# Kernel optimization log

Measured on AMD Instinct MI355X. Metric: run time of the kernel, lower is better.

The kernel has to match this reference:

```python
import jax, jax.numpy as jnp
import numpy as np

B, S, H = 1, 2048, 4096
N_HEADS, N_KV, HEAD_DIM = 32, 8, 128
ROPE_THETA = 10000.0


def setup_inputs() -> dict:
    key = jax.random.key(0)
    k1, k2, k3 = jax.random.split(key, 3)
    hidden_states = jax.random.normal(k1, (B, S, H), dtype=jnp.float32)
    # fused QKV projection weight: rows = (n_heads + 2*n_kv_heads) * head_dim
    Wqkv = jax.random.normal(k2, ((N_HEADS + 2 * N_KV) * HEAD_DIM, H), dtype=jnp.float32) * 0.02
    Wo = jax.random.normal(k3, (H, N_HEADS * HEAD_DIM), dtype=jnp.float32) * 0.02
    return {"hidden_states": hidden_states, "Wqkv": Wqkv, "Wo": Wo}


def _rope_tables(seqlen, dim, theta):
    inv_freq = 1.0 / (theta ** (jnp.arange(0, dim, 2, dtype=jnp.float32) / dim))  # [dim/2]
    t = jnp.arange(seqlen, dtype=jnp.float32)
    freqs = jnp.outer(t, inv_freq)  # [S, dim/2]
    return jnp.cos(freqs), jnp.sin(freqs)


def _apply_rope(x, cos, sin):
    # torch code: reshape(...,2,-1).transpose -> view_as_complex pairs (x[j], x[j+d/2])
    # i.e. NeoX rotate-half on first/second halves of head_dim.
    d2 = x.shape[-1] // 2
    x1, x2 = x[..., :d2], x[..., d2:]
    c = cos[None, :, None, :]  # [1,S,1,d/2]
    s = sin[None, :, None, :]
    return jnp.concatenate([x1 * c - x2 * s, x1 * s + x2 * c], axis=-1)


def reference(hidden_states, Wqkv, Wo):
    b, s, h = hidden_states.shape
    # fused QKV projection
    qkv = jnp.einsum('bsh,oh->bso', hidden_states, Wqkv)
    q_end = N_HEADS * HEAD_DIM
    k_end = q_end + N_KV * HEAD_DIM
    xq = qkv[..., :q_end].reshape(b, s, N_HEADS, HEAD_DIM)
    xk = qkv[..., q_end:k_end].reshape(b, s, N_KV, HEAD_DIM)
    xv = qkv[..., k_end:].reshape(b, s, N_KV, HEAD_DIM)
    # RoPE (start_pos = 0 prefill)
    cos, sin = _rope_tables(s, HEAD_DIM, ROPE_THETA)
    xq = _apply_rope(xq, cos, sin)
    xk = _apply_rope(xk, cos, sin)
    # GQA: expand kv heads to query heads (head h uses kv head h // groups)
    groups = N_HEADS // N_KV
    xk = jnp.repeat(xk, groups, axis=2)  # [b,s,nH,hd]
    xv = jnp.repeat(xv, groups, axis=2)
    # causal attention, softmax scale 1/sqrt(head_dim) (flash_attn default, softcap=0)
    scale = 1.0 / jnp.sqrt(jnp.float32(HEAD_DIM))
    scores = jnp.einsum('bqhd,bkhd->bhqk', xq, xk) * scale
    causal = jnp.tril(jnp.ones((s, s), dtype=bool))
    scores = jnp.where(causal[None, None, :, :], scores, jnp.float32(-1e30))
    probs = jax.nn.softmax(scores, axis=-1)
    out = jnp.einsum('bhqk,bkhd->bqhd', probs, xv).reshape(b, s, N_HEADS * HEAD_DIM)
    attn_output = jnp.einsum('bsd,hd->bsh', out, Wo)
    return attn_output
```

## Files before the change

kernel.cpp:

```cpp
#include <hip/hip_runtime.h>
#include <stdint.h>

typedef unsigned short u16;
typedef unsigned int   u32;
typedef short bf16x8 __attribute__((ext_vector_type(8)));
typedef float f32x4  __attribute__((ext_vector_type(4)));

__device__ __forceinline__ u16 f2bf(float f) {
    union { float f; u32 u; } v; v.f = f;
    u32 u = v.u;
    u32 r = (u + 0x7fffu + ((u >> 16) & 1u)) >> 16;
    return (u16)r;
}
__device__ __forceinline__ float bf2f(u16 h) {
    union { u32 u; float f; } v; v.u = ((u32)h) << 16;
    return v.f;
}

__device__ __forceinline__ void gload_lds16(const void* g, void* l) {
    __builtin_amdgcn_global_load_lds(
        (__attribute__((address_space(1))) void*)g,
        (__attribute__((address_space(3))) void*)l,
        16, 0, 0);
}

__global__ __launch_bounds__(256) void cvt_all(const float4* __restrict__ s1, uint2* __restrict__ d1,
                                               const float4* __restrict__ s2, uint2* __restrict__ d2,
                                               const float4* __restrict__ s3, uint2* __restrict__ d3) {
    const float4* s; uint2* d; int i;
    int b = blockIdx.x;
    if (b < 8192)        { s = s1; d = d1; i = b * 256 + threadIdx.x; }
    else if (b < 32768)  { s = s2; d = d2; i = (b - 8192) * 256 + threadIdx.x; }
    else                 { s = s3; d = d3; i = (b - 32768) * 256 + threadIdx.x; }
    float4 v = s[i];
    uint2 o;
    o.x = (u32)f2bf(v.x) | ((u32)f2bf(v.y) << 16);
    o.y = (u32)f2bf(v.z) | ((u32)f2bf(v.w) << 16);
    d[i] = o;
}

template <typename OUT_T>
__global__ __launch_bounds__(256) void gemm_bt(const u16* __restrict__ A,
                                               const u16* __restrict__ B,
                                               OUT_T* __restrict__ C,
                                               int M, int N, int K) {
    __shared__ u16 As[128 * 32];
    __shared__ u16 Bs[128 * 32];

    const int tid  = threadIdx.x;
    const int lane = tid & 63;
    const int wv   = tid >> 6;
    const int row0 = blockIdx.y * 128;
    const int col0 = blockIdx.x * 128;

    const int wm = (wv >> 1) * 64;
    const int wn = (wv & 1) * 64;
    const int fr = lane & 15;
    const int fq = (lane >> 4) * 8;

    const int srow = lane >> 2;
    const int scol = (lane & 3) * 8;

    f32x4 acc[4][4];
#pragma unroll
    for (int i = 0; i < 4; ++i)
#pragma unroll
        for (int j = 0; j < 4; ++j) acc[i][j] = f32x4{0.f, 0.f, 0.f, 0.f};

    for (int k0 = 0; k0 < K; k0 += 32) {
        __syncthreads();
#pragma unroll
        for (int i = 0; i < 2; ++i) {
            const int chunk = wv * 2 + i;
            const int r     = chunk * 16 + srow;
            gload_lds16(A + (size_t)(row0 + r) * K + k0 + scol, &As[r * 32 + scol]);
            gload_lds16(B + (size_t)(col0 + r) * K + k0 + scol, &Bs[r * 32 + scol]);
        }
        __syncthreads();

        bf16x8 af[4], bf[4];
#pragma unroll
        for (int mt = 0; mt < 4; ++mt)
            af[mt] = *(const bf16x8*)&As[(wm + mt * 16 + fr) * 32 + fq];
#pragma unroll
        for (int nt = 0; nt < 4; ++nt)
            bf[nt] = *(const bf16x8*)&Bs[(wn + nt * 16 + fr) * 32 + fq];
#pragma unroll
        for (int mt = 0; mt < 4; ++mt)
#pragma unroll
            for (int nt = 0; nt < 4; ++nt)
                acc[mt][nt] = __builtin_amdgcn_mfma_f32_16x16x32_bf16(
                    af[mt], bf[nt], acc[mt][nt], 0, 0, 0);
    }

    const int orow4 = (lane >> 4) * 4;
    const int ocol  = lane & 15;
#pragma unroll
    for (int mt = 0; mt < 4; ++mt)
#pragma unroll
        for (int nt = 0; nt < 4; ++nt)
#pragma unroll
            for (int r = 0; r < 4; ++r) {
                int mm = row0 + wm + mt * 16 + orow4 + r;
                int nn = col0 + wn + nt * 16 + ocol;
                float v = acc[mt][nt][r];
                if constexpr (sizeof(OUT_T) == 2)
                    C[(size_t)mm * N + nn] = (OUT_T)f2bf(v);
                else
                    C[(size_t)mm * N + nn] = (OUT_T)v;
            }
}

__global__ __launch_bounds__(256) void prep_kv(const u16* __restrict__ qkv,
                                               u16* __restrict__ Kb,
                                               u16* __restrict__ Vt) {
    if (blockIdx.x < 4096) {
        int id = blockIdx.x * 256 + threadIdx.x;
        int d  = id & 63;
        int t  = id >> 6;
        int kh = t & 7;
        int s  = t >> 3;
        const size_t rowbase = (size_t)s * 6144 + 4096;
        float inv = __expf(-(float)d * (9.210340371976184f / 64.0f));
        float ang = (float)s * inv;
        float cs, sn; __sincosf(ang, &sn, &cs);
        float x1 = bf2f(qkv[rowbase + kh * 128 + d]);
        float x2 = bf2f(qkv[rowbase + kh * 128 + d + 64]);
        size_t o = ((size_t)kh * 2048 + s) * 128 + d;
        Kb[o]      = f2bf(x1 * cs - x2 * sn);
        Kb[o + 64] = f2bf(x1 * sn + x2 * cs);
    } else {
        int id = (blockIdx.x - 4096) * 256 + threadIdx.x;
        int s8 = id & 255;
        int d  = (id >> 8) & 127;
        int vh = id >> 15;
        u16 tmp[8];
#pragma unroll
        for (int j = 0; j < 8; ++j)
            tmp[j] = qkv[(size_t)(s8 * 8 + j) * 6144 + 5120 + vh * 128 + d];
        *(uint4*)(Vt + ((size_t)vh * 128 + d) * 2048 + s8 * 8) = *(uint4*)tmp;
    }
}

__device__ __forceinline__ void attn_pass(const bf16x8 qf[4], f32x4 acc[8], float lr[4],
                                          const u16* Ks, const u16* Vs, u16* Psw,
                                          int w, int m, int quad, bool diag, float sl2e) {
    f32x4 sacc[4];
#pragma unroll
    for (int nt = 0; nt < 4; ++nt) sacc[nt] = f32x4{0.f, 0.f, 0.f, 0.f};
#pragma unroll
    for (int kk = 0; kk < 4; ++kk) {
#pragma unroll
        for (int nt = 0; nt < 4; ++nt) {
            int pos = (kk * 4 + quad) ^ (m & 7);
            bf16x8 b = *(const bf16x8*)&Ks[(nt * 16 + m) * 128 + pos * 8];
            sacc[nt] = __builtin_amdgcn_mfma_f32_16x16x32_bf16(qf[kk], b, sacc[nt], 0, 0, 0);
        }
    }

#pragma unroll
    for (int nt = 0; nt < 4; ++nt)
#pragma unroll
        for (int r = 0; r < 4; ++r) {
            float p = __builtin_amdgcn_exp2f(sacc[nt][r] * sl2e);
            if (diag && (nt * 16 + m > w * 16 + quad * 4 + r)) p = 0.f;
            sacc[nt][r] = p;
            lr[r] += p;
        }

#pragma unroll
    for (int nt = 0; nt < 4; ++nt)
#pragma unroll
        for (int r = 0; r < 4; ++r)
            Psw[(quad * 4 + r) * 72 + nt * 16 + m] = f2bf(sacc[nt][r]);

#pragma unroll
    for (int kk2 = 0; kk2 < 2; ++kk2) {
        bf16x8 a = *(const bf16x8*)&Psw[m * 72 + kk2 * 32 + quad * 8];
#pragma unroll
        for (int nt = 0; nt < 8; ++nt) {
            int n = nt * 16 + m;
            int pos = (kk2 * 4 + quad) ^ (m & 7);
            bf16x8 b = *(const bf16x8*)&Vs[n * 64 + pos * 8];
            acc[nt] = __builtin_amdgcn_mfma_f32_16x16x32_bf16(a, b, acc[nt], 0, 0, 0);
        }
    }
}

__global__ __launch_bounds__(256) void attn_mfma(const u16* __restrict__ qkv,
                                                 const u16* __restrict__ Kb,
                                                 const u16* __restrict__ Vt,
                                                 u16* __restrict__ ctx) {
    __shared__ u16 Ks[64 * 128];
    __shared__ u16 Vs[128 * 64];
    __shared__ u16 Ps[4][16 * 72];

    const int tid  = threadIdx.x;
    const int lane = tid & 63;
    const int w    = tid >> 6;
    const int m    = lane & 15;
    const int quad = lane >> 4;
    const int h    = blockIdx.y;
    const int kh   = h >> 2;
    const int qtA  = blockIdx.x;
    const int qtB  = 31 - qtA;

    const u16* Ktile0 = Kb + (size_t)kh * 2048 * 128;
    const u16* Vtile0 = Vt + (size_t)kh * 128 * 2048;
    const float sl2e = 0.08838834764831845f * 1.4426950408889634f;

    bf16x8 qa[4], qb[4];
#pragma unroll
    for (int which = 0; which < 2; ++which) {
        const int qt = which ? qtB : qtA;
        const int s  = qt * 64 + w * 16 + m;
        bf16x8 raw[4];
        const u16* qp = qkv + (size_t)s * 6144 + h * 128 + quad * 8;
#pragma unroll
        for (int kk = 0; kk < 4; ++kk)
            raw[kk] = *(const bf16x8*)(qp + kk * 32);
        bf16x8* dst = which ? qb : qa;
#pragma unroll
        for (int half = 0; half < 2; ++half)
#pragma unroll
            for (int j = 0; j < 8; ++j) {
                int d = half * 32 + quad * 8 + j;
                float inv = __expf(-(float)d * (9.210340371976184f / 64.0f));
                float ang = (float)s * inv;
                float cs, sn; __sincosf(ang, &sn, &cs);
                float x1 = bf2f(((const u16*)&raw[half])[j]);
                float x2 = bf2f(((const u16*)&raw[half + 2])[j]);
                ((u16*)&dst[half])[j]     = f2bf(x1 * cs - x2 * sn);
                ((u16*)&dst[half + 2])[j] = f2bf(x1 * sn + x2 * cs);
            }
    }

    f32x4 accA[8], accB[8];
#pragma unroll
    for (int i = 0; i < 8; ++i) { accA[i] = f32x4{0.f, 0.f, 0.f, 0.f}; accB[i] = f32x4{0.f, 0.f, 0.f, 0.f}; }
    float lA[4] = {0.f, 0.f, 0.f, 0.f};
    float lB[4] = {0.f, 0.f, 0.f, 0.f};

    for (int kt = 0; kt <= qtB; ++kt) {
        __syncthreads();
        {
            const u16* Kt = Ktile0 + (size_t)kt * 64 * 128;
#pragma unroll
            for (int i = 0; i < 4; ++i) {
                int slot = i * 256 + tid;
                int row = slot >> 4, cp = slot & 15;
                int gc = cp ^ (row & 7);
                gload_lds16(Kt + row * 128 + gc * 8, &Ks[slot * 8]);
            }
            const u16* Vtt = Vtile0 + kt * 64;
#pragma unroll
            for (int i = 0; i < 4; ++i) {
                int slot = i * 256 + tid;
                int row = slot >> 3, cp = slot & 7;
                int gc = cp ^ (row & 7);
                gload_lds16(Vtt + (size_t)row * 2048 + gc * 8, &Vs[slot * 8]);
            }
        }
        __syncthreads();

        if (kt <= qtA)
            attn_pass(qa, accA, lA, Ks, Vs, Ps[w], w, m, quad, kt == qtA, sl2e);
        attn_pass(qb, accB, lB, Ks, Vs, Ps[w], w, m, quad, kt == qtB, sl2e);
    }

#pragma unroll
    for (int which = 0; which < 2; ++which) {
        const int qt   = which ? qtB : qtA;
        f32x4*   acc   = which ? accB : accA;
        float*   lr    = which ? lB   : lA;
#pragma unroll
        for (int r = 0; r < 4; ++r) {
            float s_ = lr[r];
            s_ += __shfl_xor(s_, 1);
            s_ += __shfl_xor(s_, 2);
            s_ += __shfl_xor(s_, 4);
            s_ += __shfl_xor(s_, 8);
            lr[r] = s_;
        }
#pragma unroll
        for (int r = 0; r < 4; ++r) {
            float inv = 1.f / lr[r];
            size_t rowg = (size_t)(qt * 64 + w * 16 + quad * 4 + r);
#pragma unroll
            for (int nt = 0; nt < 8; ++nt)
                ctx[rowg * 4096 + h * 128 + nt * 16 + m] = f2bf(acc[nt][r] * inv);
        }
    }
}

extern "C" void kernel_launch(void* const* d_in, const int* in_sizes, int n_in,
                              void* d_out, int out_size, void* d_ws, size_t ws_size,
                              hipStream_t stream) {
    const float* hs   = (const float*)d_in[0];
    const float* wqkv = (const float*)d_in[1];
    const float* wo   = (const float*)d_in[2];
    float* out = (float*)d_out;

    char* ws = (char*)d_ws;
    u16* hA  = (u16*)ws;  ws += (size_t)2048 * 4096 * 2;
    u16* wQ  = (u16*)ws;  ws += (size_t)6144 * 4096 * 2;
    u16* wO  = (u16*)ws;  ws += (size_t)4096 * 4096 * 2;
    u16* qkv = (u16*)ws;  ws += (size_t)2048 * 6144 * 2;
    u16* Kb  = (u16*)ws;  ws += (size_t)8 * 2048 * 128 * 2;
    u16* Vt  = (u16*)ws;  ws += (size_t)8 * 128 * 2048 * 2;
    u16* ctx = (u16*)ws;  ws += (size_t)2048 * 4096 * 2;

    cvt_all<<<49152, 256, 0, stream>>>((const float4*)hs,   (uint2*)hA,
                                       (const float4*)wqkv, (uint2*)wQ,
                                       (const float4*)wo,   (uint2*)wO);

    gemm_bt<u16><<<dim3(48, 16), 256, 0, stream>>>(hA, wQ, qkv, 2048, 6144, 4096);

    prep_kv<<<5120, 256, 0, stream>>>(qkv, Kb, Vt);

    attn_mfma<<<dim3(16, 32), 256, 0, stream>>>(qkv, Kb, Vt, ctx);

    gemm_bt<float><<<dim3(32, 16), 256, 0, stream>>>(ctx, wO, out, 2048, 4096, 4096);
}
```

Measured before the change: 545.5 us.

## Double-buffer LDS tiles in GEMM and attention to overlap loads with MFMA

Both the bf16 GEMM and the attention kernel now keep two LDS buffers for the A/B (or K/V) tiles. The next tile's global-to-LDS async loads are issued right after a single barrier, before computing on the current buffer, so each iteration needs one barrier instead of two. The aim is to hide global memory latency behind the MFMA work. The cost is twice the LDS footprint, which may lower occupancy, especially in attention (about 73KB per block). The overlap may also be lost if the compiler inserts a full vmcnt wait before the LDS reads.

```diff
diff --git a/kernel.cpp b/kernel.cpp
--- a/kernel.cpp
+++ b/kernel.cpp
@@ -44,8 +44,8 @@
                                                const u16* __restrict__ B,
                                                OUT_T* __restrict__ C,
                                                int M, int N, int K) {
-    __shared__ u16 As[128 * 32];
-    __shared__ u16 Bs[128 * 32];
+    __shared__ u16 As[2][128 * 32];
+    __shared__ u16 Bs[2][128 * 32];
 
     const int tid  = threadIdx.x;
     const int lane = tid & 63;
@@ -67,24 +67,32 @@
 #pragma unroll
         for (int j = 0; j < 4; ++j) acc[i][j] = f32x4{0.f, 0.f, 0.f, 0.f};
 
-    for (int k0 = 0; k0 < K; k0 += 32) {
-        __syncthreads();
+    auto stage = [&](int buf, int k0) {
 #pragma unroll
         for (int i = 0; i < 2; ++i) {
             const int chunk = wv * 2 + i;
             const int r     = chunk * 16 + srow;
-            gload_lds16(A + (size_t)(row0 + r) * K + k0 + scol, &As[r * 32 + scol]);
-            gload_lds16(B + (size_t)(col0 + r) * K + k0 + scol, &Bs[r * 32 + scol]);
-        }
+            gload_lds16(A + (size_t)(row0 + r) * K + k0 + scol, &As[buf][r * 32 + scol]);
+            gload_lds16(B + (size_t)(col0 + r) * K + k0 + scol, &Bs[buf][r * 32 + scol]);
+        }
+    };
+
+    const int nk = K >> 5;
+    stage(0, 0);
+
+    for (int ki = 0; ki < nk; ++ki) {
         __syncthreads();
-
+        if (ki + 1 < nk) stage((ki + 1) & 1, (ki + 1) << 5);
+
+        const u16* as = As[ki & 1];
+        const u16* bs = Bs[ki & 1];
         bf16x8 af[4], bf[4];
 #pragma unroll
         for (int mt = 0; mt < 4; ++mt)
-            af[mt] = *(const bf16x8*)&As[(wm + mt * 16 + fr) * 32 + fq];
+            af[mt] = *(const bf16x8*)&as[(wm + mt * 16 + fr) * 32 + fq];
 #pragma unroll
         for (int nt = 0; nt < 4; ++nt)
-            bf[nt] = *(const bf16x8*)&Bs[(wn + nt * 16 + fr) * 32 + fq];
+            bf[nt] = *(const bf16x8*)&bs[(wn + nt * 16 + fr) * 32 + fq];
 #pragma unroll
         for (int mt = 0; mt < 4; ++mt)
 #pragma unroll
@@ -191,8 +199,8 @@
                                                  const u16* __restrict__ Kb,
                                                  const u16* __restrict__ Vt,
                                                  u16* __restrict__ ctx) {
-    __shared__ u16 Ks[64 * 128];
-    __shared__ u16 Vs[128 * 64];
+    __shared__ u16 Ks[2][64 * 128];
+    __shared__ u16 Vs[2][128 * 64];
     __shared__ u16 Ps[4][16 * 72];
 
     const int tid  = threadIdx.x;
@@ -208,6 +216,25 @@
     const u16* Ktile0 = Kb + (size_t)kh * 2048 * 128;
     const u16* Vtile0 = Vt + (size_t)kh * 128 * 2048;
     const float sl2e = 0.08838834764831845f * 1.4426950408889634f;
+
+    auto stage = [&](int buf, int kt) {
+        const u16* Kt = Ktile0 + (size_t)kt * 64 * 128;
+#pragma unroll
+        for (int i = 0; i < 4; ++i) {
+            int slot = i * 256 + tid;
+            int row = slot >> 4, cp = slot & 15;
+            int gc = cp ^ (row & 7);
+            gload_lds16(Kt + row * 128 + gc * 8, &Ks[buf][slot * 8]);
+        }
+        const u16* Vtt = Vtile0 + kt * 64;
+#pragma unroll
+        for (int i = 0; i < 4; ++i) {
+            int slot = i * 256 + tid;
+            int row = slot >> 3, cp = slot & 7;
+            int gc = cp ^ (row & 7);
+            gload_lds16(Vtt + (size_t)row * 2048 + gc * 8, &Vs[buf][slot * 8]);
+        }
+    };
 
     bf16x8 qa[4], qb[4];
 #pragma unroll
@@ -241,31 +268,16 @@
     float lA[4] = {0.f, 0.f, 0.f, 0.f};
     float lB[4] = {0.f, 0.f, 0.f, 0.f};
 
+    stage(0, 0);
     for (int kt = 0; kt <= qtB; ++kt) {
         __syncthreads();
-        {
-            const u16* Kt = Ktile0 + (size_t)kt * 64 * 128;
-#pragma unroll
-            for (int i = 0; i < 4; ++i) {
-                int slot = i * 256 + tid;
-                int row = slot >> 4, cp = slot & 15;
-                int gc = cp ^ (row & 7);
-                gload_lds16(Kt + row * 128 + gc * 8, &Ks[slot * 8]);
-            }
-            const u16* Vtt = Vtile0 + kt * 64;
-#pragma unroll
-            for (int i = 0; i < 4; ++i) {
-                int slot = i * 256 + tid;
-                int row = slot >> 3, cp = slot & 7;
-                int gc = cp ^ (row & 7);
-                gload_lds16(Vtt + (size_t)row * 2048 + gc * 8, &Vs[slot * 8]);
-            }
-        }
-        __syncthreads();
-
+        if (kt < qtB) stage((kt + 1) & 1, kt + 1);
+
+        const u16* ks = Ks[kt & 1];
+        const u16* vs = Vs[kt & 1];
         if (kt <= qtA)
-            attn_pass(qa, accA, lA, Ks, Vs, Ps[w], w, m, quad, kt == qtA, sl2e);
-        attn_pass(qb, accB, lB, Ks, Vs, Ps[w], w, m, quad, kt == qtB, sl2e);
+            attn_pass(qa, accA, lA, ks, vs, Ps[w], w, m, quad, kt == qtA, sl2e);
+        attn_pass(qb, accB, lB, ks, vs, Ps[w], w, m, quad, kt == qtB, sl2e);
     }
 
 #pragma unroll
```

New measurement: 511.1 us. 6.3% less time.
